# Performance work log

Measured on AMD Instinct MI355X. Metric: run time of the kernel, lower is better.

Reference implementation:

```python
import jax, jax.numpy as jnp
import numpy as np
import math

B, C, L = 16, 2048, 64

def setup_inputs() -> dict:
    key = jax.random.key(0)
    kq, kk, kv = jax.random.split(key, 3)
    q = jax.random.normal(kq, (B, C, L), dtype=jnp.float32)
    k = jax.random.normal(kk, (B, C, L), dtype=jnp.float32)
    v = jax.random.normal(kv, (B, C, L), dtype=jnp.float32)
    return {"q": q, "k": k, "v": v}

def reference(q, k, v):
    b, c, l = q.shape
    # Faithful to the torch source: k is RESHAPED (row-major), not transposed.
    k_t = k.reshape(b, l, c)                      # (b, l, c)
    score = jnp.matmul(q, k_t) / math.sqrt(l)     # (b, c, c)
    # nn.Softmax() with no dim on a 3D tensor -> torch implicit dim = 0 (batch axis)
    score = jax.nn.softmax(score, axis=0)
    return jnp.matmul(score, v)                   # (b, c, l)
```

## Files before the change

kernel.cpp:

```cpp
#include <hip/hip_runtime.h>

typedef __attribute__((ext_vector_type(8))) short short8;
typedef __attribute__((ext_vector_type(4))) float float4v;

#define BATCH 16
#define CDIM 2048
#define LDIM 64
#define BSTRIDE (CDIM * LDIM)

#if __has_builtin(__builtin_amdgcn_exp2f)
#define EXPW(x) __builtin_amdgcn_exp2f(x)
#define QSCALE 0.18033688011112042f
#else
#define EXPW(x) __expf(x)
#define QSCALE 0.125f
#endif

__device__ __forceinline__ float bf2f(unsigned short u) {
    return __uint_as_float(((unsigned int)u) << 16);
}
__device__ __forceinline__ unsigned short f2bf(float f) {
    unsigned int x = __float_as_uint(f);
    x += 0x7fffu + ((x >> 16) & 1u);
    return (unsigned short)(x >> 16);
}
__device__ __forceinline__ void dma16(const void* g, void* l) {
    __builtin_amdgcn_global_load_lds(
        (const __attribute__((address_space(1))) void*)g,
        (__attribute__((address_space(3))) void*)l, 16, 0, 0);
}

__global__ __launch_bounds__(256) void prepass_kernel(
    const float* __restrict__ q, const float* __restrict__ k, const float* __restrict__ v,
    unsigned short* __restrict__ qb,
    unsigned short* __restrict__ kT, unsigned short* __restrict__ vS)
{
    __shared__ unsigned short T[64][68];
    const int bx = blockIdx.x;
    const int t = threadIdx.x;

    if (bx < 1024) {
        int i = bx * 256 + t;
        const float4v* src = (const float4v*)q + (size_t)i * 2;
        float4v x0 = src[0], x1 = src[1];
        unsigned int u0 = f2bf(x0[0] * QSCALE) | ((unsigned)f2bf(x0[1] * QSCALE) << 16);
        unsigned int u1 = f2bf(x0[2] * QSCALE) | ((unsigned)f2bf(x0[3] * QSCALE) << 16);
        unsigned int u2 = f2bf(x1[0] * QSCALE) | ((unsigned)f2bf(x1[1] * QSCALE) << 16);
        unsigned int u3 = f2bf(x1[2] * QSCALE) | ((unsigned)f2bf(x1[3] * QSCALE) << 16);
        int b = i >> 14, r = i & 16383, m = r >> 3, j = r & 7;
        *(uint4*)(qb + (size_t)b * BSTRIDE + m * 64 + (j ^ (m & 7)) * 8) =
            make_uint4(u0, u1, u2, u3);
    } else if (bx < 1536) {
        int idx = bx - 1024, b = idx >> 5, n0 = (idx & 31) * 64;
        const float* src = k + (size_t)b * BSTRIDE + (size_t)(t >> 2) * 2048 + n0 + (t & 3) * 16;
#pragma unroll
        for (int kk = 0; kk < 4; kk++) {
            float4v x = *(const float4v*)(src + kk * 4);
#pragma unroll
            for (int e = 0; e < 4; e++)
                T[t >> 2][(t & 3) * 16 + kk * 4 + e] = f2bf(x[e]);
        }
        __syncthreads();
        unsigned short* dst = kT + (size_t)b * BSTRIDE;
        int n = t & 63;
#pragma unroll
        for (int jj = 0; jj < 2; jj++) {
            int j = (t >> 6) * 2 + jj;
            ushort4 g0, g1;
#pragma unroll
            for (int e = 0; e < 4; e++) { g0[e] = T[j * 8 + e][n]; g1[e] = T[j * 8 + 4 + e][n]; }
            *(uint4*)(dst + (size_t)(n0 + n) * 64 + (j ^ (n & 7)) * 8) =
                make_uint4(g0.x | ((unsigned)g0.y << 16), g0.z | ((unsigned)g0.w << 16),
                           g1.x | ((unsigned)g1.y << 16), g1.z | ((unsigned)g1.w << 16));
        }
    } else {
        int idx = bx - 1536, b = idx >> 5, n0 = (idx & 31) * 64;
        const float* src = v + (size_t)b * BSTRIDE + (size_t)n0 * 64 +
                           (size_t)(t >> 2) * 64 + (t & 3) * 16;
#pragma unroll
        for (int kk = 0; kk < 4; kk++) {
            float4v x = *(const float4v*)(src + kk * 4);
#pragma unroll
            for (int e = 0; e < 4; e++)
                T[t >> 2][(t & 3) * 16 + kk * 4 + e] = f2bf(x[e]);
        }
        __syncthreads();
        unsigned short* dst = vS + (size_t)b * BSTRIDE;
        int j = t & 63, qc = t >> 6;
        int sw = qc ^ (j & 3) ^ ((j >> 2) & 3);
#pragma unroll
        for (int nb = 0; nb < 2; nb++) {
            ushort4 g0, g1;
#pragma unroll
            for (int e = 0; e < 4; e++) {
                g0[e] = T[nb * 32 + qc * 8 + e][j];
                g1[e] = T[nb * 32 + qc * 8 + 4 + e][j];
            }
            *(uint4*)(dst + (size_t)(n0 / 32 + nb) * 2048 + j * 32 + sw * 8) =
                make_uint4(g0.x | ((unsigned)g0.y << 16), g0.z | ((unsigned)g0.w << 16),
                           g1.x | ((unsigned)g1.y << 16), g1.z | ((unsigned)g1.w << 16));
        }
    }
}

__global__ __launch_bounds__(256, 3) void dinv_kernel(
    const unsigned short* __restrict__ qb, const unsigned short* __restrict__ kT,
    unsigned short* __restrict__ Dt)
{
    __shared__ __align__(16) unsigned char smem[49152];

    const int tid = threadIdx.x, w = tid >> 6, lane = tid & 63;
    const int c = lane & 15, q = lane >> 4;
    const int mtB = blockIdx.x & 15, ng = blockIdx.x >> 4;
    const int m0 = mtB * 128, n0 = ng * 64;

    float4v Dacc[2][4];
#pragma unroll
    for (int ms = 0; ms < 2; ms++)
#pragma unroll
        for (int nt = 0; nt < 4; nt++) Dacc[ms][nt] = (float4v){0.f, 0.f, 0.f, 0.f};

    {
        const char* qg = (const char*)(qb + (size_t)m0 * 64);
        const char* kg = (const char*)(kT + (size_t)n0 * 64);
#pragma unroll
        for (int kk = 0; kk < 4; kk++)
            dma16(qg + (w * 4 + kk) * 1024 + lane * 16, (char*)smem + (w * 4 + kk) * 1024);
        dma16(kg + (w * 2 + 0) * 1024 + lane * 16, (char*)smem + 32768 + (w * 2 + 0) * 1024);
        dma16(kg + (w * 2 + 1) * 1024 + lane * 16, (char*)smem + 32768 + (w * 2 + 1) * 1024);
    }

    for (int bb = 0; bb < BATCH; bb++) {
        const int p = bb & 1;
        asm volatile("s_waitcnt vmcnt(0)" ::: "memory");
        asm volatile("s_barrier" ::: "memory");
        if (bb < BATCH - 1) {
            const char* qg = (const char*)(qb + (size_t)(bb + 1) * BSTRIDE + (size_t)m0 * 64);
            const char* kg = (const char*)(kT + (size_t)(bb + 1) * BSTRIDE + (size_t)n0 * 64);
#pragma unroll
            for (int kk = 0; kk < 4; kk++)
                dma16(qg + (w * 4 + kk) * 1024 + lane * 16,
                      (char*)smem + (p ^ 1) * 16384 + (w * 4 + kk) * 1024);
            dma16(kg + (w * 2 + 0) * 1024 + lane * 16,
                  (char*)smem + 32768 + (p ^ 1) * 8192 + (w * 2 + 0) * 1024);
            dma16(kg + (w * 2 + 1) * 1024 + lane * 16,
                  (char*)smem + 32768 + (p ^ 1) * 8192 + (w * 2 + 1) * 1024);
        }
        const char* sq = (const char*)smem + p * 16384;
        const char* sk = (const char*)smem + 32768 + p * 8192;
        short8 Qf[2][2];
#pragma unroll
        for (int ms = 0; ms < 2; ms++)
#pragma unroll
            for (int h = 0; h < 2; h++)
                Qf[ms][h] = *(const short8*)(sq + (w * 32 + ms * 16 + c) * 128 +
                                             ((h * 4 + q) ^ (c & 7)) * 16);
#pragma unroll
        for (int nt = 0; nt < 4; nt++) {
            short8 A0 = *(const short8*)(sk + (nt * 16 + c) * 128 + ((q) ^ (c & 7)) * 16);
            short8 A1 = *(const short8*)(sk + (nt * 16 + c) * 128 + ((4 + q) ^ (c & 7)) * 16);
#pragma unroll
            for (int ms = 0; ms < 2; ms++) {
                float4v d = (float4v){0.f, 0.f, 0.f, 0.f};
                d = __builtin_amdgcn_mfma_f32_16x16x32_bf16(A0, Qf[ms][0], d, 0, 0, 0);
                d = __builtin_amdgcn_mfma_f32_16x16x32_bf16(A1, Qf[ms][1], d, 0, 0, 0);
#pragma unroll
                for (int r = 0; r < 4; r++) Dacc[ms][nt][r] += EXPW(d[r]);
            }
        }
    }

#pragma unroll
    for (int ms = 0; ms < 2; ms++)
#pragma unroll
        for (int nt = 0; nt < 4; nt++) {
            unsigned int x = f2bf(__builtin_amdgcn_rcpf(Dacc[ms][nt][0])) |
                             ((unsigned)f2bf(__builtin_amdgcn_rcpf(Dacc[ms][nt][1])) << 16);
            unsigned int y = f2bf(__builtin_amdgcn_rcpf(Dacc[ms][nt][2])) |
                             ((unsigned)f2bf(__builtin_amdgcn_rcpf(Dacc[ms][nt][3])) << 16);
            size_t tm = (size_t)(mtB * 8 + w * 2 + ms);
            size_t tp = (size_t)(ng * 2 + (nt >> 1));
            *(uint2*)((char*)Dt + (tm * 64 + tp) * 1024 + c * 64 + q * 16 + (nt & 1) * 8) =
                make_uint2(x, y);
        }
}

__global__ __launch_bounds__(512, 4) void attn_main_kernel(
    const unsigned short* __restrict__ qb, const unsigned short* __restrict__ kT,
    const unsigned short* __restrict__ vS, const unsigned short* __restrict__ Dt,
    float* __restrict__ out)
{
    __shared__ __align__(16) unsigned char smem[65536];

    const int tid = threadIdx.x, w = tid >> 6, lane = tid & 63;
    const int c = lane & 15, q = lane >> 4;
    const int g = w >> 2, ns = w & 3;
    const int b = blockIdx.x & 15, mt = blockIdx.x >> 4;
    const int m0 = mt * 64;
    const int nbase = ns * 512;

    const unsigned short* qb_b = qb + (size_t)b * BSTRIDE;
    const char* kbase = (const char*)(kT + (size_t)b * BSTRIDE);
    const char* vbase = (const char*)(vS + (size_t)b * BSTRIDE);
    char* skb = (char*)smem + ns * 8192;
    char* svb = (char*)smem + 32768 + ns * 8192;

    short8 Qf[2][2];
#pragma unroll
    for (int ms = 0; ms < 2; ms++)
#pragma unroll
        for (int h = 0; h < 2; h++)
            Qf[ms][h] = *(const short8*)(qb_b + (m0 + g * 32 + ms * 16 + c) * 64 +
                                         ((h * 4 + q) ^ (c & 7)) * 8);
    float4v acc[2][4];
#pragma unroll
    for (int ms = 0; ms < 2; ms++)
#pragma unroll
        for (int jt = 0; jt < 4; jt++) acc[ms][jt] = (float4v){0.f, 0.f, 0.f, 0.f};

    const char* dtw0 = (const char*)Dt +
        ((size_t)(mt * 4 + g * 2 + 0) * 64 + ns * 16) * 1024 + c * 64 + q * 16;
    const char* dtw1 = dtw0 + (size_t)64 * 1024;

    dma16(kbase + (size_t)nbase * 128 + (2 * g + 0) * 1024 + lane * 16, skb + (2 * g + 0) * 1024);
    dma16(kbase + (size_t)nbase * 128 + (2 * g + 1) * 1024 + lane * 16, skb + (2 * g + 1) * 1024);
    dma16(vbase + (size_t)(ns * 16) * 4096 + (2 * g + 0) * 1024 + lane * 16, svb + (2 * g + 0) * 1024);
    dma16(vbase + (size_t)(ns * 16) * 4096 + (2 * g + 1) * 1024 + lane * 16, svb + (2 * g + 1) * 1024);
    uint4 du[2];
    du[0] = *(const uint4*)(dtw0);
    du[1] = *(const uint4*)(dtw1);

    for (int st = 0; st < 16; st++) {
        const int p = st & 1;
        asm volatile("s_waitcnt vmcnt(0)" ::: "memory");
        asm volatile("s_barrier" ::: "memory");

        uint4 nu[2] = {du[0], du[1]};
        if (st < 15) {
            const int n1 = nbase + (st + 1) * 32;
            dma16(kbase + (size_t)n1 * 128 + (2 * g + 0) * 1024 + lane * 16,
                  skb + (p ^ 1) * 4096 + (2 * g + 0) * 1024);
            dma16(kbase + (size_t)n1 * 128 + (2 * g + 1) * 1024 + lane * 16,
                  skb + (p ^ 1) * 4096 + (2 * g + 1) * 1024);
            dma16(vbase + (size_t)(ns * 16 + st + 1) * 4096 + (2 * g + 0) * 1024 + lane * 16,
                  svb + (p ^ 1) * 4096 + (2 * g + 0) * 1024);
            dma16(vbase + (size_t)(ns * 16 + st + 1) * 4096 + (2 * g + 1) * 1024 + lane * 16,
                  svb + (p ^ 1) * 4096 + (2 * g + 1) * 1024);
            nu[0] = *(const uint4*)(dtw0 + (size_t)(st + 1) * 1024);
            nu[1] = *(const uint4*)(dtw1 + (size_t)(st + 1) * 1024);
        }

        const char* skp = skb + p * 4096;
        unsigned int pr[2][2][2];
#pragma unroll
        for (int nt = 0; nt < 2; nt++) {
            short8 A0 = *(const short8*)(skp + (nt * 16 + c) * 128 + ((q) ^ (c & 7)) * 16);
            short8 A1 = *(const short8*)(skp + (nt * 16 + c) * 128 + ((4 + q) ^ (c & 7)) * 16);
#pragma unroll
            for (int ms = 0; ms < 2; ms++) {
                float4v d = (float4v){0.f, 0.f, 0.f, 0.f};
                d = __builtin_amdgcn_mfma_f32_16x16x32_bf16(A0, Qf[ms][0], d, 0, 0, 0);
                d = __builtin_amdgcn_mfma_f32_16x16x32_bf16(A1, Qf[ms][1], d, 0, 0, 0);
                unsigned int ux = nt ? du[ms].z : du[ms].x;
                unsigned int uy = nt ? du[ms].w : du[ms].y;
                float p0 = EXPW(d[0]) * __uint_as_float(ux << 16);
                float p1 = EXPW(d[1]) * __uint_as_float(ux & 0xffff0000u);
                float p2 = EXPW(d[2]) * __uint_as_float(uy << 16);
                float p3 = EXPW(d[3]) * __uint_as_float(uy & 0xffff0000u);
                pr[ms][nt][0] = f2bf(p0) | ((unsigned)f2bf(p1) << 16);
                pr[ms][nt][1] = f2bf(p2) | ((unsigned)f2bf(p3) << 16);
            }
        }

        union PU { unsigned int i[4]; short8 s; };
        PU pu0, pu1;
#pragma unroll
        for (int t = 0; t < 4; t++) {
            int src = (2 * (q & 1) + (t >> 1)) * 16 + c;
            int a0 = __shfl((int)pr[0][0][t & 1], src);
            int b0 = __shfl((int)pr[0][1][t & 1], src);
            pu0.i[t] = (unsigned int)((q >= 2) ? b0 : a0);
            int a1 = __shfl((int)pr[1][0][t & 1], src);
            int b1 = __shfl((int)pr[1][1][t & 1], src);
            pu1.i[t] = (unsigned int)((q >= 2) ? b1 : a1);
        }

        const char* svp = svb + p * 4096;
#pragma unroll
        for (int jt = 0; jt < 4; jt++) {
            short8 Vf = *(const short8*)(svp + (jt * 16 + c) * 64 +
                                         ((q ^ (c & 3) ^ ((c >> 2) & 3))) * 16);
            acc[0][jt] = __builtin_amdgcn_mfma_f32_16x16x32_bf16(pu0.s, Vf, acc[0][jt], 0, 0, 0);
            acc[1][jt] = __builtin_amdgcn_mfma_f32_16x16x32_bf16(pu1.s, Vf, acc[1][jt], 0, 0, 0);
        }
        du[0] = nu[0]; du[1] = nu[1];
    }

    __syncthreads();
    {
        float* cpy = (float*)((char*)smem + (ns & 1) * 17408);
        if (ns < 2) {
#pragma unroll
            for (int ms = 0; ms < 2; ms++)
#pragma unroll
                for (int jt = 0; jt < 4; jt++)
#pragma unroll
                    for (int r = 0; r < 4; r++)
                        cpy[(g * 32 + ms * 16 + q * 4 + r) * 68 + jt * 16 + c] = acc[ms][jt][r];
        }
    }
    __syncthreads();
    {
        float* cpy = (float*)((char*)smem + (ns & 1) * 17408);
        if (ns >= 2) {
#pragma unroll
            for (int ms = 0; ms < 2; ms++)
#pragma unroll
                for (int jt = 0; jt < 4; jt++)
#pragma unroll
                    for (int r = 0; r < 4; r++)
                        cpy[(g * 32 + ms * 16 + q * 4 + r) * 68 + jt * 16 + c] += acc[ms][jt][r];
        }
    }
    __syncthreads();
    {
        int ml = tid >> 3, j0 = (tid & 7) * 8;
        const float* c0 = (const float*)smem + ml * 68 + j0;
        const float* c1 = (const float*)((char*)smem + 17408) + ml * 68 + j0;
        float4v s0 = *(const float4v*)c0 + *(const float4v*)c1;
        float4v s1 = *(const float4v*)(c0 + 4) + *(const float4v*)(c1 + 4);
        float* dst = out + ((size_t)b * CDIM + m0 + ml) * LDIM + j0;
        *(float4v*)dst = s0;
        *(float4v*)(dst + 4) = s1;
    }
}

extern "C" void kernel_launch(void* const* d_in, const int* in_sizes, int n_in,
                              void* d_out, int out_size, void* d_ws, size_t ws_size,
                              hipStream_t stream) {
    const float* q = (const float*)d_in[0];
    const float* k = (const float*)d_in[1];
    const float* v = (const float*)d_in[2];
    float* out = (float*)d_out;

    unsigned short* qb = (unsigned short*)d_ws;
    unsigned short* kT = qb + (size_t)BATCH * BSTRIDE;
    unsigned short* vS = kT + (size_t)BATCH * BSTRIDE;
    unsigned short* Dt = vS + (size_t)BATCH * BSTRIDE;

    prepass_kernel<<<2048, 256, 0, stream>>>(q, k, v, qb, kT, vS);
    dinv_kernel<<<512, 256, 0, stream>>>(qb, kT, Dt);
    attn_main_kernel<<<512, 512, 0, stream>>>(qb, kT, vS, Dt, out);
}
```

Baseline: 126.6 us.

## Move V conversion into dinv kernel and use packed bf16 convert

The V fp32-to-bf16 swizzle work moves out of the prepass kernel and becomes extra blocks of the dinv kernel, so it runs alongside the denominator computation instead of before it. All float-to-bf16 pair conversions now go through a packed hardware convert builtin when one is available, in place of manual round-to-nearest bit manipulation. This includes the hot P conversion in the main attention loop. The transpose staging buffers now hold fp32 values, which doubles their LDS footprint. The builtin's rounding may differ slightly from the manual version.

```diff
diff --git a/kernel.cpp b/kernel.cpp
--- a/kernel.cpp
+++ b/kernel.cpp
@@ -24,6 +24,18 @@
     x += 0x7fffu + ((x >> 16) & 1u);
     return (unsigned short)(x >> 16);
 }
+#if __has_builtin(__builtin_amdgcn_cvt_pk_bf16_f32)
+__device__ __forceinline__ unsigned int pk2bf(float a, float b) {
+    auto t = __builtin_amdgcn_cvt_pk_bf16_f32(a, b);
+    unsigned int u;
+    __builtin_memcpy(&u, &t, 4);
+    return u;
+}
+#else
+__device__ __forceinline__ unsigned int pk2bf(float a, float b) {
+    return f2bf(a) | ((unsigned)f2bf(b) << 16);
+}
+#endif
 __device__ __forceinline__ void dma16(const void* g, void* l) {
     __builtin_amdgcn_global_load_lds(
         (const __attribute__((address_space(1))) void*)g,
@@ -31,11 +43,10 @@
 }
 
 __global__ __launch_bounds__(256) void prepass_kernel(
-    const float* __restrict__ q, const float* __restrict__ k, const float* __restrict__ v,
-    unsigned short* __restrict__ qb,
-    unsigned short* __restrict__ kT, unsigned short* __restrict__ vS)
+    const float* __restrict__ q, const float* __restrict__ k,
+    unsigned short* __restrict__ qb, unsigned short* __restrict__ kT)
 {
-    __shared__ unsigned short T[64][68];
+    __shared__ float T[64][68];
     const int bx = blockIdx.x;
     const int t = threadIdx.x;
 
@@ -43,14 +54,14 @@
         int i = bx * 256 + t;
         const float4v* src = (const float4v*)q + (size_t)i * 2;
         float4v x0 = src[0], x1 = src[1];
-        unsigned int u0 = f2bf(x0[0] * QSCALE) | ((unsigned)f2bf(x0[1] * QSCALE) << 16);
-        unsigned int u1 = f2bf(x0[2] * QSCALE) | ((unsigned)f2bf(x0[3] * QSCALE) << 16);
-        unsigned int u2 = f2bf(x1[0] * QSCALE) | ((unsigned)f2bf(x1[1] * QSCALE) << 16);
-        unsigned int u3 = f2bf(x1[2] * QSCALE) | ((unsigned)f2bf(x1[3] * QSCALE) << 16);
+        unsigned int u0 = pk2bf(x0[0] * QSCALE, x0[1] * QSCALE);
+        unsigned int u1 = pk2bf(x0[2] * QSCALE, x0[3] * QSCALE);
+        unsigned int u2 = pk2bf(x1[0] * QSCALE, x1[1] * QSCALE);
+        unsigned int u3 = pk2bf(x1[2] * QSCALE, x1[3] * QSCALE);
         int b = i >> 14, r = i & 16383, m = r >> 3, j = r & 7;
         *(uint4*)(qb + (size_t)b * BSTRIDE + m * 64 + (j ^ (m & 7)) * 8) =
             make_uint4(u0, u1, u2, u3);
-    } else if (bx < 1536) {
+    } else {
         int idx = bx - 1024, b = idx >> 5, n0 = (idx & 31) * 64;
         const float* src = k + (size_t)b * BSTRIDE + (size_t)(t >> 2) * 2048 + n0 + (t & 3) * 16;
 #pragma unroll
@@ -58,7 +69,7 @@
             float4v x = *(const float4v*)(src + kk * 4);
 #pragma unroll
             for (int e = 0; e < 4; e++)
-                T[t >> 2][(t & 3) * 16 + kk * 4 + e] = f2bf(x[e]);
+                T[t >> 2][(t & 3) * 16 + kk * 4 + e] = x[e];
         }
         __syncthreads();
         unsigned short* dst = kT + (size_t)b * BSTRIDE;
@@ -66,50 +77,52 @@
 #pragma unroll
         for (int jj = 0; jj < 2; jj++) {
             int j = (t >> 6) * 2 + jj;
-            ushort4 g0, g1;
-#pragma unroll
-            for (int e = 0; e < 4; e++) { g0[e] = T[j * 8 + e][n]; g1[e] = T[j * 8 + 4 + e][n]; }
             *(uint4*)(dst + (size_t)(n0 + n) * 64 + (j ^ (n & 7)) * 8) =
-                make_uint4(g0.x | ((unsigned)g0.y << 16), g0.z | ((unsigned)g0.w << 16),
-                           g1.x | ((unsigned)g1.y << 16), g1.z | ((unsigned)g1.w << 16));
-        }
-    } else {
-        int idx = bx - 1536, b = idx >> 5, n0 = (idx & 31) * 64;
-        const float* src = v + (size_t)b * BSTRIDE + (size_t)n0 * 64 +
-                           (size_t)(t >> 2) * 64 + (t & 3) * 16;
-#pragma unroll
-        for (int kk = 0; kk < 4; kk++) {
-            float4v x = *(const float4v*)(src + kk * 4);
-#pragma unroll
-            for (int e = 0; e < 4; e++)
-                T[t >> 2][(t & 3) * 16 + kk * 4 + e] = f2bf(x[e]);
-        }
-        __syncthreads();
-        unsigned short* dst = vS + (size_t)b * BSTRIDE;
-        int j = t & 63, qc = t >> 6;
-        int sw = qc ^ (j & 3) ^ ((j >> 2) & 3);
-#pragma unroll
-        for (int nb = 0; nb < 2; nb++) {
-            ushort4 g0, g1;
-#pragma unroll
-            for (int e = 0; e < 4; e++) {
-                g0[e] = T[nb * 32 + qc * 8 + e][j];
-                g1[e] = T[nb * 32 + qc * 8 + 4 + e][j];
-            }
-            *(uint4*)(dst + (size_t)(n0 / 32 + nb) * 2048 + j * 32 + sw * 8) =
-                make_uint4(g0.x | ((unsigned)g0.y << 16), g0.z | ((unsigned)g0.w << 16),
-                           g1.x | ((unsigned)g1.y << 16), g1.z | ((unsigned)g1.w << 16));
-        }
-    }
-}
-
-__global__ __launch_bounds__(256, 3) void dinv_kernel(
+                make_uint4(pk2bf(T[j * 8 + 0][n], T[j * 8 + 1][n]),
+                           pk2bf(T[j * 8 + 2][n], T[j * 8 + 3][n]),
+                           pk2bf(T[j * 8 + 4][n], T[j * 8 + 5][n]),
+                           pk2bf(T[j * 8 + 6][n], T[j * 8 + 7][n]));
+        }
+    }
+}
+
+__global__ __launch_bounds__(256, 3) void dinv_vpre_kernel(
     const unsigned short* __restrict__ qb, const unsigned short* __restrict__ kT,
+    const float* __restrict__ v, unsigned short* __restrict__ vS,
     unsigned short* __restrict__ Dt)
 {
     __shared__ __align__(16) unsigned char smem[49152];
 
-    const int tid = threadIdx.x, w = tid >> 6, lane = tid & 63;
+    const int tid = threadIdx.x;
+
+    if (blockIdx.x >= 512) {
+        float (*T)[68] = (float(*)[68])smem;
+        int idx = blockIdx.x - 512, b = idx >> 5, n0 = (idx & 31) * 64;
+        const float* src = v + (size_t)b * BSTRIDE + (size_t)n0 * 64 +
+                           (size_t)(tid >> 2) * 64 + (tid & 3) * 16;
+#pragma unroll
+        for (int kk = 0; kk < 4; kk++) {
+            float4v x = *(const float4v*)(src + kk * 4);
+#pragma unroll
+            for (int e = 0; e < 4; e++)
+                T[tid >> 2][(tid & 3) * 16 + kk * 4 + e] = x[e];
+        }
+        __syncthreads();
+        unsigned short* dst = vS + (size_t)b * BSTRIDE;
+        int j = tid & 63, qc = tid >> 6;
+        int sw = qc ^ (j & 3) ^ ((j >> 2) & 3);
+#pragma unroll
+        for (int nb = 0; nb < 2; nb++) {
+            *(uint4*)(dst + (size_t)(n0 / 32 + nb) * 2048 + j * 32 + sw * 8) =
+                make_uint4(pk2bf(T[nb * 32 + qc * 8 + 0][j], T[nb * 32 + qc * 8 + 1][j]),
+                           pk2bf(T[nb * 32 + qc * 8 + 2][j], T[nb * 32 + qc * 8 + 3][j]),
+                           pk2bf(T[nb * 32 + qc * 8 + 4][j], T[nb * 32 + qc * 8 + 5][j]),
+                           pk2bf(T[nb * 32 + qc * 8 + 6][j], T[nb * 32 + qc * 8 + 7][j]));
+        }
+        return;
+    }
+
+    const int w = tid >> 6, lane = tid & 63;
     const int c = lane & 15, q = lane >> 4;
     const int mtB = blockIdx.x & 15, ng = blockIdx.x >> 4;
     const int m0 = mtB * 128, n0 = ng * 64;
@@ -174,10 +187,10 @@
     for (int ms = 0; ms < 2; ms++)
 #pragma unroll
         for (int nt = 0; nt < 4; nt++) {
-            unsigned int x = f2bf(__builtin_amdgcn_rcpf(Dacc[ms][nt][0])) |
-                             ((unsigned)f2bf(__builtin_amdgcn_rcpf(Dacc[ms][nt][1])) << 16);
-            unsigned int y = f2bf(__builtin_amdgcn_rcpf(Dacc[ms][nt][2])) |
-                             ((unsigned)f2bf(__builtin_amdgcn_rcpf(Dacc[ms][nt][3])) << 16);
+            unsigned int x = pk2bf(__builtin_amdgcn_rcpf(Dacc[ms][nt][0]),
+                                   __builtin_amdgcn_rcpf(Dacc[ms][nt][1]));
+            unsigned int y = pk2bf(__builtin_amdgcn_rcpf(Dacc[ms][nt][2]),
+                                   __builtin_amdgcn_rcpf(Dacc[ms][nt][3]));
             size_t tm = (size_t)(mtB * 8 + w * 2 + ms);
             size_t tp = (size_t)(ng * 2 + (nt >> 1));
             *(uint2*)((char*)Dt + (tm * 64 + tp) * 1024 + c * 64 + q * 16 + (nt & 1) * 8) =
@@ -263,12 +276,10 @@
                 d = __builtin_amdgcn_mfma_f32_16x16x32_bf16(A1, Qf[ms][1], d, 0, 0, 0);
                 unsigned int ux = nt ? du[ms].z : du[ms].x;
                 unsigned int uy = nt ? du[ms].w : du[ms].y;
-                float p0 = EXPW(d[0]) * __uint_as_float(ux << 16);
-                float p1 = EXPW(d[1]) * __uint_as_float(ux & 0xffff0000u);
-                float p2 = EXPW(d[2]) * __uint_as_float(uy << 16);
-                float p3 = EXPW(d[3]) * __uint_as_float(uy & 0xffff0000u);
-                pr[ms][nt][0] = f2bf(p0) | ((unsigned)f2bf(p1) << 16);
-                pr[ms][nt][1] = f2bf(p2) | ((unsigned)f2bf(p3) << 16);
+                pr[ms][nt][0] = pk2bf(EXPW(d[0]) * __uint_as_float(ux << 16),
+                                      EXPW(d[1]) * __uint_as_float(ux & 0xffff0000u));
+                pr[ms][nt][1] = pk2bf(EXPW(d[2]) * __uint_as_float(uy << 16),
+                                      EXPW(d[3]) * __uint_as_float(uy & 0xffff0000u));
             }
         }
 
@@ -348,7 +359,7 @@
     unsigned short* vS = kT + (size_t)BATCH * BSTRIDE;
     unsigned short* Dt = vS + (size_t)BATCH * BSTRIDE;
 
-    prepass_kernel<<<2048, 256, 0, stream>>>(q, k, v, qb, kT, vS);
-    dinv_kernel<<<512, 256, 0, stream>>>(qb, kT, Dt);
+    prepass_kernel<<<1536, 256, 0, stream>>>(q, k, qb, kT);
+    dinv_vpre_kernel<<<1024, 256, 0, stream>>>(qb, kT, v, vS, Dt);
     attn_main_kernel<<<512, 512, 0, stream>>>(qb, kT, vS, Dt, out);
 }
```

Measured after the change: 124.1 us. 2.0% less time.
